# Kernel optimization log

Measured on AMD Instinct MI355X. Metric: run time of the kernel, lower is better.

## Reference

```python
import jax, jax.numpy as jnp
import numpy as np

B, S, D, H = 2, 2048, 1024, 16
HD = D // H  # head_features = 64
MASKED_BIAS = -10000.0


def setup_inputs() -> dict:
    key = jax.random.key(0)
    ks = jax.random.split(key, 5)
    return {
        "hidden_states": jax.random.normal(ks[0], (B, S, D), dtype=jnp.float32),
        "c_attn_w": jax.random.normal(ks[1], (D, 3 * D), dtype=jnp.float32) * 0.02,
        "c_attn_b": jax.random.normal(ks[2], (3 * D,), dtype=jnp.float32) * 0.02,
        "c_proj_w": jax.random.normal(ks[3], (D, D), dtype=jnp.float32) * 0.02,
        "c_proj_b": jax.random.normal(ks[4], (D,), dtype=jnp.float32) * 0.02,
    }


def reference(hidden_states, c_attn_w, c_attn_b, c_proj_w, c_proj_b):
    b, s, d = hidden_states.shape
    # Conv1D: x @ W + b, projecting D -> 3D, then split into q, k, v
    qkv = hidden_states @ c_attn_w + c_attn_b  # [b, s, 3D]
    q, k, v = jnp.split(qkv, 3, axis=-1)
    # split heads -> [b, H, s, HD]
    q = q.reshape(b, s, H, HD).transpose(0, 2, 1, 3)
    k = k.reshape(b, s, H, HD).transpose(0, 2, 1, 3)
    v = v.reshape(b, s, H, HD).transpose(0, 2, 1, 3)
    # scaled scores: [b, H, s, s]
    w = jnp.einsum("bhqd,bhkd->bhqk", q, k) / jnp.sqrt(jnp.float32(HD))
    # causal mask (tril bias buffer) applied via where with masked_bias
    causal = jnp.tril(jnp.ones((s, s), dtype=bool))
    w = jnp.where(causal[None, None], w, jnp.float32(MASKED_BIAS))
    p = jax.nn.softmax(w, axis=-1)  # attn_dropout p=0
    a = jnp.einsum("bhqk,bhkd->bhqd", p, v)  # [b, H, s, HD]
    # merge heads -> [b, s, D], output projection (resid_dropout p=0)
    a = a.transpose(0, 2, 1, 3).reshape(b, s, d)
    return a @ c_proj_w + c_proj_b
```

## Files before the change

### kernel.cpp

```cpp
#include <hip/hip_runtime.h>

typedef unsigned short u16;
typedef unsigned int   u32;

typedef __attribute__((ext_vector_type(8))) short bf16x8;
typedef __attribute__((ext_vector_type(4))) short bf16x4;
typedef __attribute__((ext_vector_type(4))) float f32x4;

typedef const __attribute__((address_space(1))) u32 gq_t;
typedef __attribute__((address_space(3))) u32 lq_t;

__device__ __forceinline__ float b2f(u16 u) {
    union { u32 u; float f; } c; c.u = ((u32)u) << 16; return c.f;
}
__device__ __forceinline__ u16 f2b(float f) {
    union { float f; u32 u; } c; c.f = f;
    u32 r = c.u + 0x7fffu + ((c.u >> 16) & 1u);
    return (u16)(r >> 16);
}
__device__ __forceinline__ u16 f2b_hu(float f) {
    union { float f; u32 u; } c; c.f = f;
    return (u16)((c.u + 0x8000u) >> 16);
}

__global__ __launch_bounds__(256) void prep(
    const float* __restrict__ X,    u16* __restrict__ Xb,
    const float* __restrict__ Wqkv, u16* __restrict__ WqkvT,
    const float* __restrict__ Wp,   u16* __restrict__ WprojT)
{
    __shared__ float t[32][33];
    const int bid = blockIdx.x, tid = threadIdx.x;
    if (bid < 2048) {
        const int i = (bid * 256 + tid) * 8;
        f32x4 a = *(const f32x4*)(X + i);
        f32x4 b = *(const f32x4*)(X + i + 4);
        union { bf16x8 v; u16 u[8]; } o;
        o.u[0] = f2b(a[0]); o.u[1] = f2b(a[1]); o.u[2] = f2b(a[2]); o.u[3] = f2b(a[3]);
        o.u[4] = f2b(b[0]); o.u[5] = f2b(b[1]); o.u[6] = f2b(b[2]); o.u[7] = f2b(b[3]);
        *(bf16x8*)(Xb + i) = o.v;
        return;
    }
    const float* in; u16* out; int N, bx, by;
    if (bid < 5120) { const int b2 = bid - 2048; in = Wqkv; out = WqkvT; N = 3072; bx = b2 % 96; by = b2 / 96; }
    else            { const int b3 = bid - 5120; in = Wp;   out = WprojT; N = 1024; bx = b3 & 31; by = b3 >> 5; }
    const int k0 = by * 32, n0 = bx * 32;
    const int kr = tid >> 3, nc = (tid & 7) * 4;
    f32x4 v = *(const f32x4*)(in + (size_t)(k0 + kr) * N + n0 + nc);
    t[kr][nc] = v[0]; t[kr][nc + 1] = v[1]; t[kr][nc + 2] = v[2]; t[kr][nc + 3] = v[3];
    __syncthreads();
    const int nr = tid >> 3, kc = (tid & 7) * 4;
    union { bf16x4 v; u16 a[4]; } o;
    o.a[0] = f2b(t[kc][nr]);     o.a[1] = f2b(t[kc + 1][nr]);
    o.a[2] = f2b(t[kc + 2][nr]); o.a[3] = f2b(t[kc + 3][nr]);
    *(bf16x4*)(out + (size_t)(n0 + nr) * 1024 + k0 + kc) = o.v;
}

__global__ __launch_bounds__(256) void gemm128(
    const u16* __restrict__ A, const u16* __restrict__ WT,
    const float* __restrict__ bias, float* __restrict__ out,
    u16* __restrict__ Qb, u16* __restrict__ Kb, u16* __restrict__ Vt,
    int N, int K, int mode)
{
    __shared__ u16 As[128 * 64];
    __shared__ u16 Bs[128 * 64];
    const int tid  = threadIdx.x;
    const int m0   = blockIdx.y * 128, n0 = blockIdx.x * 128;
    const int wv   = tid >> 6, lane = tid & 63;
    const int wm   = (wv >> 1) * 64, wn = (wv & 1) * 64;
    const int l16  = lane & 15, quad = lane >> 4;

    const int srow = tid >> 3;
    const int slog = ((tid & 7) ^ (srow & 7)) * 8;
    const int rsw8 = l16 & 7;

    f32x4 acc[4][4];
    const f32x4 zero = {0.f, 0.f, 0.f, 0.f};
    #pragma unroll
    for (int i = 0; i < 4; i++)
        #pragma unroll
        for (int j = 0; j < 4; j++) acc[i][j] = zero;

    for (int k0 = 0; k0 < K; k0 += 64) {
        #pragma unroll
        for (int c = 0; c < 4; c++) {
            const u16* ag = A  + (size_t)(m0 + c * 32 + srow) * K + k0 + slog;
            const u16* bg = WT + (size_t)(n0 + c * 32 + srow) * K + k0 + slog;
            __builtin_amdgcn_global_load_lds((gq_t*)ag, (lq_t*)&As[c * 2048 + wv * 512], 16, 0, 0);
            __builtin_amdgcn_global_load_lds((gq_t*)bg, (lq_t*)&Bs[c * 2048 + wv * 512], 16, 0, 0);
        }
        __syncthreads();
        #pragma unroll
        for (int ks = 0; ks < 2; ks++) {
            const int ph = (((ks * 4 + quad) ^ rsw8) * 8);
            bf16x8 af[4], bfr[4];
            #pragma unroll
            for (int i = 0; i < 4; i++) {
                af[i]  = *(const bf16x8*)&As[(wm + i * 16 + l16) * 64 + ph];
                bfr[i] = *(const bf16x8*)&Bs[(wn + i * 16 + l16) * 64 + ph];
            }
            #pragma unroll
            for (int i = 0; i < 4; i++)
                #pragma unroll
                for (int j = 0; j < 4; j++)
                    acc[i][j] = __builtin_amdgcn_mfma_f32_16x16x32_bf16(af[i], bfr[j], acc[i][j], 0, 0, 0);
        }
        __syncthreads();
    }

    #pragma unroll
    for (int j = 0; j < 4; j++) {
        const int nn = n0 + wn + j * 16 + l16;
        const float bvf = bias[nn];
        #pragma unroll
        for (int i = 0; i < 4; i++) {
            float o[4];
            #pragma unroll
            for (int r = 0; r < 4; r++) o[r] = acc[i][j][r] + bvf;
            const int mbase = m0 + wm + i * 16 + quad * 4;
            if (mode == 0) {
                #pragma unroll
                for (int r = 0; r < 4; r++)
                    out[(size_t)(mbase + r) * N + nn] = o[r];
            } else {
                const int part = nn >> 10, w = nn & 1023;
                const int h = w >> 6, d = w & 63;
                const int b = mbase >> 11, s = mbase & 2047;
                const size_t bh = (size_t)b * 16 + h;
                if (part == 2) {
                    union { bf16x4 v; u16 a[4]; } pk;
                    #pragma unroll
                    for (int r = 0; r < 4; r++) pk.a[r] = f2b_hu(o[r]);
                    *(bf16x4*)(Vt + (bh * 64 + d) * 2048 + s) = pk.v;
                } else {
                    u16* t = (part == 0) ? Qb : Kb;
                    const float scl = (part == 0) ? 0.125f : 1.0f;
                    #pragma unroll
                    for (int r = 0; r < 4; r++)
                        t[(bh * 2048 + s + r) * 64 + d] = f2b_hu(o[r] * scl);
                }
            }
        }
    }
}

__global__ __launch_bounds__(256) void gemm_proj(
    const u16* __restrict__ A, const u16* __restrict__ WT,
    const float* __restrict__ bias, float* __restrict__ out, int N, int K)
{
    __shared__ u16 As[128 * 32];
    __shared__ u16 Bs[64 * 32];
    const int tid  = threadIdx.x;
    const int m0   = blockIdx.y * 128, n0 = blockIdx.x * 64;
    const int wv   = tid >> 6, lane = tid & 63;
    const int wm   = (wv >> 1) * 64, wn = (wv & 1) * 32;
    const int l16  = lane & 15, quad = lane >> 4;

    const int sr = lane >> 2;
    const int sc = (((lane & 3) ^ ((lane >> 3) & 3)) * 8);
    const int rbase = wv * 16 + sr;
    const int rsw = ((l16 >> 1) & 3) * 8;

    f32x4 acc[4][2];
    const f32x4 zero = {0.f, 0.f, 0.f, 0.f};
    #pragma unroll
    for (int i = 0; i < 4; i++) { acc[i][0] = zero; acc[i][1] = zero; }

    for (int k0 = 0; k0 < K; k0 += 32) {
        #pragma unroll
        for (int c = 0; c < 2; c++) {
            const u16* ag = A + (size_t)(m0 + c * 64 + rbase) * K + k0 + sc;
            __builtin_amdgcn_global_load_lds((gq_t*)ag, (lq_t*)&As[(c * 64 + wv * 16) * 32], 16, 0, 0);
        }
        const u16* bg = WT + (size_t)(n0 + rbase) * K + k0 + sc;
        __builtin_amdgcn_global_load_lds((gq_t*)bg, (lq_t*)&Bs[(wv * 16) * 32], 16, 0, 0);
        __syncthreads();
        bf16x8 af[4], bfr[2];
        #pragma unroll
        for (int i = 0; i < 4; i++)
            af[i] = *(const bf16x8*)&As[(wm + i * 16 + l16) * 32 + ((quad * 8) ^ rsw)];
        #pragma unroll
        for (int j = 0; j < 2; j++)
            bfr[j] = *(const bf16x8*)&Bs[(wn + j * 16 + l16) * 32 + ((quad * 8) ^ rsw)];
        #pragma unroll
        for (int i = 0; i < 4; i++)
            #pragma unroll
            for (int j = 0; j < 2; j++)
                acc[i][j] = __builtin_amdgcn_mfma_f32_16x16x32_bf16(af[i], bfr[j], acc[i][j], 0, 0, 0);
        __syncthreads();
    }

    #pragma unroll
    for (int j = 0; j < 2; j++) {
        const int nn = n0 + wn + j * 16 + l16;
        const float bvf = bias[nn];
        #pragma unroll
        for (int i = 0; i < 4; i++) {
            const int mbase = m0 + wm + i * 16 + quad * 4;
            #pragma unroll
            for (int r = 0; r < 4; r++)
                out[(size_t)(mbase + r) * N + nn] = acc[i][j][r] + bvf;
        }
    }
}

__global__ __launch_bounds__(256, 4) void attn_mfma(
    const u16* __restrict__ Qb, const u16* __restrict__ Kb,
    const u16* __restrict__ Vt, u16* __restrict__ Aout)
{
    const int bx   = blockIdx.x;
    const int x    = bx & 511, half = bx >> 9;
    const int xcd  = x & 7, y = x >> 3;
    const int bh   = xcd * 4 + (y & 3);
    const int pidx = y >> 2;
    const int chunk = half ? (31 - pidx) : pidx;
    const int q0   = chunk * 64;

    const int tid  = threadIdx.x;
    const int wave = tid >> 6, lane = tid & 63;
    const int l16  = lane & 15, quad = lane >> 4;
    const int qw   = q0 + wave * 16;
    const size_t kbase = (size_t)bh * 2048 * 64;
    const size_t vbase = (size_t)bh * 64 * 2048;

    __shared__ __align__(16) u16 Ks[64 * 72];
    __shared__ __align__(16) u16 Vs[64 * 72];
    __shared__ __align__(16) u16 p_all[4][16 * 72];
    u16* p_lds = p_all[wave];

    const u16* qp = Qb + kbase + (size_t)(qw + l16) * 64 + quad * 8;
    bf16x8 aq0 = *(const bf16x8*)qp;
    bf16x8 aq1 = *(const bf16x8*)(qp + 32);

    union { bf16x8 v; u16 a[8]; } onesu;
    #pragma unroll
    for (int j = 0; j < 8; j++) onesu.a[j] = 0x3F80;
    const bf16x8 vones = onesu.v;

    f32x4 oacc[4], lacc;
    const f32x4 zero = {0.f, 0.f, 0.f, 0.f};
    #pragma unroll
    for (int t = 0; t < 4; t++) oacc[t] = zero;
    lacc = zero;

    const int srow = tid >> 2, scol = (tid & 3) * 16;
    u16* ksw = &Ks[srow * 72 + scol];
    u16* vsw = &Vs[srow * 72 + scol];

    {
        const u16* kg = Kb + kbase + (size_t)srow * 64 + scol;
        const u16* vg = Vt + vbase + (size_t)srow * 2048 + scol;
        bf16x8 k0 = *(const bf16x8*)kg, k1 = *(const bf16x8*)(kg + 8);
        bf16x8 v0 = *(const bf16x8*)vg, v1 = *(const bf16x8*)(vg + 8);
        *(bf16x8*)ksw = k0; *(bf16x8*)(ksw + 8) = k1;
        *(bf16x8*)vsw = v0; *(bf16x8*)(vsw + 8) = v1;
    }
    __syncthreads();

    for (int kt = 0; kt <= chunk; kt++) {
        const int kb = kt * 64;
        const bool pf = (kt < chunk);

        bf16x8 pk0, pk1, pv0, pv1;
        if (pf) {
            const u16* kg = Kb + kbase + (size_t)(kb + 64 + srow) * 64 + scol;
            const u16* vg = Vt + vbase + (size_t)srow * 2048 + (kb + 64) + scol;
            pk0 = *(const bf16x8*)kg; pk1 = *(const bf16x8*)(kg + 8);
            pv0 = *(const bf16x8*)vg; pv1 = *(const bf16x8*)(vg + 8);
        }

        bf16x8 kk[8], vv[8];
        #pragma unroll
        for (int t = 0; t < 4; t++) {
            #pragma unroll
            for (int ks = 0; ks < 2; ks++) {
                kk[2 * t + ks] = *(const bf16x8*)&Ks[(16 * t + l16) * 72 + ks * 32 + quad * 8];
                vv[2 * t + ks] = *(const bf16x8*)&Vs[(16 * t + l16) * 72 + ks * 32 + quad * 8];
            }
        }

        f32x4 sc[4];
        #pragma unroll
        for (int t = 0; t < 4; t++) {
            sc[t] = __builtin_amdgcn_mfma_f32_16x16x32_bf16(aq0, kk[2 * t],     zero,  0, 0, 0);
            sc[t] = __builtin_amdgcn_mfma_f32_16x16x32_bf16(aq1, kk[2 * t + 1], sc[t], 0, 0, 0);
        }

        const bool diag = (kt == chunk);
        #pragma unroll
        for (int r = 0; r < 4; r++) {
            const int qi = qw + quad * 4 + r;
            u16* pw = &p_lds[(quad * 4 + r) * 72 + l16];
            #pragma unroll
            for (int t = 0; t < 4; t++) {
                float pv = __expf(sc[t][r]);
                if (diag && (kb + 16 * t + l16 > qi)) pv = 0.f;
                pw[16 * t] = f2b_hu(pv);
            }
        }

        __asm__ volatile("s_waitcnt lgkmcnt(0)");

        #pragma unroll
        for (int ks = 0; ks < 2; ks++) {
            bf16x8 ap = *(const bf16x8*)&p_lds[l16 * 72 + ks * 32 + quad * 8];
            #pragma unroll
            for (int t = 0; t < 4; t++)
                oacc[t] = __builtin_amdgcn_mfma_f32_16x16x32_bf16(ap, vv[2 * t + ks], oacc[t], 0, 0, 0);
            lacc = __builtin_amdgcn_mfma_f32_16x16x32_bf16(ap, vones, lacc, 0, 0, 0);
        }

        __syncthreads();
        if (pf) {
            *(bf16x8*)ksw = pk0; *(bf16x8*)(ksw + 8) = pk1;
            *(bf16x8*)vsw = pv0; *(bf16x8*)(vsw + 8) = pv1;
            __syncthreads();
        }
    }

    const int b = bh >> 4, h = bh & 15;
    #pragma unroll
    for (int r = 0; r < 4; r++) {
        const float inv = 1.0f / lacc[r];
        const int qi = qw + quad * 4 + r;
        u16* dst = Aout + (size_t)(b * 2048 + qi) * 1024 + h * 64 + l16;
        #pragma unroll
        for (int t = 0; t < 4; t++)
            dst[16 * t] = f2b_hu(oacc[t][r] * inv);
    }
}

extern "C" void kernel_launch(void* const* d_in, const int* in_sizes, int n_in,
                              void* d_out, int out_size, void* d_ws, size_t ws_size,
                              hipStream_t stream)
{
    const float* X    = (const float*)d_in[0];
    const float* Wqkv = (const float*)d_in[1];
    const float* Bqkv = (const float*)d_in[2];
    const float* Wp   = (const float*)d_in[3];
    const float* Bp   = (const float*)d_in[4];
    float* out = (float*)d_out;

    char* ws = (char*)d_ws;
    u16* WqkvT = (u16*)(ws);
    u16* WprojT= (u16*)(ws + 6291456);
    u16* Qb    = (u16*)(ws + 8388608);
    u16* Kb    = (u16*)(ws + 16777216);
    u16* Vt    = (u16*)(ws + 25165824);
    u16* Ab    = (u16*)(ws + 33554432);
    u16* Xb    = (u16*)(ws + 41943040);

    prep<<<dim3(6144), 256, 0, stream>>>(X, Xb, Wqkv, WqkvT, Wp, WprojT);

    gemm128<<<dim3(24, 32), 256, 0, stream>>>(Xb, WqkvT, Bqkv, nullptr,
                                              Qb, Kb, Vt, 3072, 1024, 1);
    attn_mfma<<<dim3(1024), 256, 0, stream>>>(Qb, Kb, Vt, Ab);
    gemm_proj<<<dim3(16, 32), 256, 0, stream>>>(Ab, WprojT, Bp, out, 1024, 1024);
}
```

Baseline: 172.9 us.

## Double-buffer K/V tiles via direct global-to-LDS loads with XOR swizzle

The attention kernel now stages K and V tiles straight from global memory into LDS with global_load_lds into two buffers, replacing the register-staged single buffer. This drops the second barrier per iteration and lets the next tile's loads overlap compute. The padded LDS rows are replaced by an XOR-swizzled 64-wide layout for K, V and P to avoid bank conflicts. Q is pre-scaled by log2(e)/8 so the softmax can use exp2f instead of __expf. The code relies on the async LDS loads having landed before the single barrier, which could be a correctness risk.

```diff
diff --git a/kernel.cpp b/kernel.cpp
--- a/kernel.cpp
+++ b/kernel.cpp
@@ -22,6 +22,8 @@
     union { float f; u32 u; } c; c.f = f;
     return (u16)((c.u + 0x8000u) >> 16);
 }
+
+#define QSCALE 0.18033688011112042f
 
 __global__ __launch_bounds__(256) void prep(
     const float* __restrict__ X,    u16* __restrict__ Xb,
@@ -133,7 +135,7 @@
                     *(bf16x4*)(Vt + (bh * 64 + d) * 2048 + s) = pk.v;
                 } else {
                     u16* t = (part == 0) ? Qb : Kb;
-                    const float scl = (part == 0) ? 0.125f : 1.0f;
+                    const float scl = (part == 0) ? QSCALE : 1.0f;
                     #pragma unroll
                     for (int r = 0; r < 4; r++)
                         t[(bh * 2048 + s + r) * 64 + d] = f2b_hu(o[r] * scl);
@@ -222,9 +224,9 @@
     const size_t kbase = (size_t)bh * 2048 * 64;
     const size_t vbase = (size_t)bh * 64 * 2048;
 
-    __shared__ __align__(16) u16 Ks[64 * 72];
-    __shared__ __align__(16) u16 Vs[64 * 72];
-    __shared__ __align__(16) u16 p_all[4][16 * 72];
+    __shared__ __align__(16) u16 Ks[2][64 * 64];
+    __shared__ __align__(16) u16 Vs[2][64 * 64];
+    __shared__ __align__(16) u16 p_all[4][16 * 64];
     u16* p_lds = p_all[wave];
 
     const u16* qp = Qb + kbase + (size_t)(qw + l16) * 64 + quad * 8;
@@ -242,39 +244,40 @@
     for (int t = 0; t < 4; t++) oacc[t] = zero;
     lacc = zero;
 
-    const int srow = tid >> 2, scol = (tid & 3) * 16;
-    u16* ksw = &Ks[srow * 72 + scol];
-    u16* vsw = &Vs[srow * 72 + scol];
-
-    {
-        const u16* kg = Kb + kbase + (size_t)srow * 64 + scol;
-        const u16* vg = Vt + vbase + (size_t)srow * 2048 + scol;
-        bf16x8 k0 = *(const bf16x8*)kg, k1 = *(const bf16x8*)(kg + 8);
-        bf16x8 v0 = *(const bf16x8*)vg, v1 = *(const bf16x8*)(vg + 8);
-        *(bf16x8*)ksw = k0; *(bf16x8*)(ksw + 8) = k1;
-        *(bf16x8*)vsw = v0; *(bf16x8*)(vsw + 8) = v1;
-    }
+    const int drow = lane >> 3;
+    const int dcol = ((lane & 7) ^ drow) * 8;
+    const int r0a = wave * 16, r0b = wave * 16 + 8;
+
+    #define STAGE(nb, kbt)                                                              \
+    {                                                                                   \
+        const u16* kga = Kb + kbase + (size_t)((kbt) + r0a + drow) * 64 + dcol;         \
+        const u16* kgb = Kb + kbase + (size_t)((kbt) + r0b + drow) * 64 + dcol;         \
+        const u16* vga = Vt + vbase + (size_t)(r0a + drow) * 2048 + (kbt) + dcol;       \
+        const u16* vgb = Vt + vbase + (size_t)(r0b + drow) * 2048 + (kbt) + dcol;       \
+        __builtin_amdgcn_global_load_lds((gq_t*)kga, (lq_t*)&Ks[nb][r0a * 64], 16, 0, 0);\
+        __builtin_amdgcn_global_load_lds((gq_t*)kgb, (lq_t*)&Ks[nb][r0b * 64], 16, 0, 0);\
+        __builtin_amdgcn_global_load_lds((gq_t*)vga, (lq_t*)&Vs[nb][r0a * 64], 16, 0, 0);\
+        __builtin_amdgcn_global_load_lds((gq_t*)vgb, (lq_t*)&Vs[nb][r0b * 64], 16, 0, 0);\
+    }
+
+    STAGE(0, 0)
     __syncthreads();
 
+    const int swk = l16 & 7;
     for (int kt = 0; kt <= chunk; kt++) {
-        const int kb = kt * 64;
-        const bool pf = (kt < chunk);
-
-        bf16x8 pk0, pk1, pv0, pv1;
-        if (pf) {
-            const u16* kg = Kb + kbase + (size_t)(kb + 64 + srow) * 64 + scol;
-            const u16* vg = Vt + vbase + (size_t)srow * 2048 + (kb + 64) + scol;
-            pk0 = *(const bf16x8*)kg; pk1 = *(const bf16x8*)(kg + 8);
-            pv0 = *(const bf16x8*)vg; pv1 = *(const bf16x8*)(vg + 8);
-        }
-
+        const int kb = kt * 64, buf = kt & 1;
+        if (kt < chunk) STAGE(buf ^ 1, kb + 64)
+
+        const u16* Kl = Ks[buf];
+        const u16* Vl = Vs[buf];
         bf16x8 kk[8], vv[8];
         #pragma unroll
         for (int t = 0; t < 4; t++) {
             #pragma unroll
             for (int ks = 0; ks < 2; ks++) {
-                kk[2 * t + ks] = *(const bf16x8*)&Ks[(16 * t + l16) * 72 + ks * 32 + quad * 8];
-                vv[2 * t + ks] = *(const bf16x8*)&Vs[(16 * t + l16) * 72 + ks * 32 + quad * 8];
+                const int ph = ((ks * 4 + quad) ^ swk) * 8;
+                kk[2 * t + ks] = *(const bf16x8*)&Kl[(16 * t + l16) * 64 + ph];
+                vv[2 * t + ks] = *(const bf16x8*)&Vl[(16 * t + l16) * 64 + ph];
             }
         }
 
@@ -288,13 +291,15 @@
         const bool diag = (kt == chunk);
         #pragma unroll
         for (int r = 0; r < 4; r++) {
-            const int qi = qw + quad * 4 + r;
-            u16* pw = &p_lds[(quad * 4 + r) * 72 + l16];
+            const int row = quad * 4 + r;
+            const int qi = qw + row;
+            u16* pw = &p_lds[row * 64 + (l16 & 7)];
+            const int rk = row & 7;
             #pragma unroll
             for (int t = 0; t < 4; t++) {
-                float pv = __expf(sc[t][r]);
+                float pv = exp2f(sc[t][r]);
                 if (diag && (kb + 16 * t + l16 > qi)) pv = 0.f;
-                pw[16 * t] = f2b_hu(pv);
+                pw[(((2 * t + (l16 >> 3)) ^ rk) * 8)] = f2b_hu(pv);
             }
         }
 
@@ -302,7 +307,7 @@
 
         #pragma unroll
         for (int ks = 0; ks < 2; ks++) {
-            bf16x8 ap = *(const bf16x8*)&p_lds[l16 * 72 + ks * 32 + quad * 8];
+            bf16x8 ap = *(const bf16x8*)&p_lds[l16 * 64 + (((ks * 4 + quad) ^ swk) * 8)];
             #pragma unroll
             for (int t = 0; t < 4; t++)
                 oacc[t] = __builtin_amdgcn_mfma_f32_16x16x32_bf16(ap, vv[2 * t + ks], oacc[t], 0, 0, 0);
@@ -310,11 +315,6 @@
         }
 
         __syncthreads();
-        if (pf) {
-            *(bf16x8*)ksw = pk0; *(bf16x8*)(ksw + 8) = pk1;
-            *(bf16x8*)vsw = pv0; *(bf16x8*)(vsw + 8) = pv1;
-            __syncthreads();
-        }
     }
 
     const int b = bh >> 4, h = bh & 15;
@@ -327,6 +327,7 @@
         for (int t = 0; t < 4; t++)
             dst[16 * t] = f2b_hu(oacc[t][r] * inv);
     }
+    #undef STAGE
 }
 
 extern "C" void kernel_launch(void* const* d_in, const int* in_sizes, int n_in,
```

Measured after the change: 184.0 us. 6.5% more time.

## Load K/V fragments directly from global memory, drop LDS staging and barriers

Applied to the files above, without the earlier changes.

The attention kernel no longer stages K and V tiles through shared memory with block-wide barriers. Each wave now loads its MFMA operand fragments straight from global memory (relying on L2/L1 caching across the four waves). The softmax also switches from __expf to exp2f, with log2(e) folded into the Q scale in the QKV GEMM epilogue. This removes two __syncthreads per iteration and the LDS round trip, at the cost of four times more global/cache traffic and losing the explicit prefetch of the next tile.

```diff
diff --git a/kernel.cpp b/kernel.cpp
--- a/kernel.cpp
+++ b/kernel.cpp
@@ -22,6 +22,8 @@
     union { float f; u32 u; } c; c.f = f;
     return (u16)((c.u + 0x8000u) >> 16);
 }
+
+#define QSCALE 0.18033688011112042f
 
 __global__ __launch_bounds__(256) void prep(
     const float* __restrict__ X,    u16* __restrict__ Xb,
@@ -133,7 +135,7 @@
                     *(bf16x4*)(Vt + (bh * 64 + d) * 2048 + s) = pk.v;
                 } else {
                     u16* t = (part == 0) ? Qb : Kb;
-                    const float scl = (part == 0) ? 0.125f : 1.0f;
+                    const float scl = (part == 0) ? QSCALE : 1.0f;
                     #pragma unroll
                     for (int r = 0; r < 4; r++)
                         t[(bh * 2048 + s + r) * 64 + d] = f2b_hu(o[r] * scl);
@@ -222,8 +224,6 @@
     const size_t kbase = (size_t)bh * 2048 * 64;
     const size_t vbase = (size_t)bh * 64 * 2048;
 
-    __shared__ __align__(16) u16 Ks[64 * 72];
-    __shared__ __align__(16) u16 Vs[64 * 72];
     __shared__ __align__(16) u16 p_all[4][16 * 72];
     u16* p_lds = p_all[wave];
 
@@ -242,40 +242,21 @@
     for (int t = 0; t < 4; t++) oacc[t] = zero;
     lacc = zero;
 
-    const int srow = tid >> 2, scol = (tid & 3) * 16;
-    u16* ksw = &Ks[srow * 72 + scol];
-    u16* vsw = &Vs[srow * 72 + scol];
-
-    {
-        const u16* kg = Kb + kbase + (size_t)srow * 64 + scol;
-        const u16* vg = Vt + vbase + (size_t)srow * 2048 + scol;
-        bf16x8 k0 = *(const bf16x8*)kg, k1 = *(const bf16x8*)(kg + 8);
-        bf16x8 v0 = *(const bf16x8*)vg, v1 = *(const bf16x8*)(vg + 8);
-        *(bf16x8*)ksw = k0; *(bf16x8*)(ksw + 8) = k1;
-        *(bf16x8*)vsw = v0; *(bf16x8*)(vsw + 8) = v1;
-    }
-    __syncthreads();
+    const u16* kp0 = Kb + kbase + (size_t)l16 * 64 + quad * 8;
+    const u16* vp0 = Vt + vbase + (size_t)l16 * 2048 + quad * 8;
 
     for (int kt = 0; kt <= chunk; kt++) {
         const int kb = kt * 64;
-        const bool pf = (kt < chunk);
-
-        bf16x8 pk0, pk1, pv0, pv1;
-        if (pf) {
-            const u16* kg = Kb + kbase + (size_t)(kb + 64 + srow) * 64 + scol;
-            const u16* vg = Vt + vbase + (size_t)srow * 2048 + (kb + 64) + scol;
-            pk0 = *(const bf16x8*)kg; pk1 = *(const bf16x8*)(kg + 8);
-            pv0 = *(const bf16x8*)vg; pv1 = *(const bf16x8*)(vg + 8);
-        }
 
         bf16x8 kk[8], vv[8];
         #pragma unroll
         for (int t = 0; t < 4; t++) {
-            #pragma unroll
-            for (int ks = 0; ks < 2; ks++) {
-                kk[2 * t + ks] = *(const bf16x8*)&Ks[(16 * t + l16) * 72 + ks * 32 + quad * 8];
-                vv[2 * t + ks] = *(const bf16x8*)&Vs[(16 * t + l16) * 72 + ks * 32 + quad * 8];
-            }
+            const u16* kp = kp0 + (size_t)(kb + 16 * t) * 64;
+            kk[2 * t]     = *(const bf16x8*)kp;
+            kk[2 * t + 1] = *(const bf16x8*)(kp + 32);
+            const u16* vp = vp0 + (size_t)(16 * t) * 2048 + kb;
+            vv[2 * t]     = *(const bf16x8*)vp;
+            vv[2 * t + 1] = *(const bf16x8*)(vp + 32);
         }
 
         f32x4 sc[4];
@@ -292,7 +273,7 @@
             u16* pw = &p_lds[(quad * 4 + r) * 72 + l16];
             #pragma unroll
             for (int t = 0; t < 4; t++) {
-                float pv = __expf(sc[t][r]);
+                float pv = exp2f(sc[t][r]);
                 if (diag && (kb + 16 * t + l16 > qi)) pv = 0.f;
                 pw[16 * t] = f2b_hu(pv);
             }
@@ -307,13 +288,6 @@
             for (int t = 0; t < 4; t++)
                 oacc[t] = __builtin_amdgcn_mfma_f32_16x16x32_bf16(ap, vv[2 * t + ks], oacc[t], 0, 0, 0);
             lacc = __builtin_amdgcn_mfma_f32_16x16x32_bf16(ap, vones, lacc, 0, 0, 0);
-        }
-
-        __syncthreads();
-        if (pf) {
-            *(bf16x8*)ksw = pk0; *(bf16x8*)(ksw + 8) = pk1;
-            *(bf16x8*)vsw = pv0; *(bf16x8*)(vsw + 8) = pv1;
-            __syncthreads();
         }
     }
 
```

Measured after the change: 260.4 us. +50.7%, slower.
